# Optimization experiments

Hardware: AMD Instinct MI355X
Metric: run time of the kernel (lower is better)

Reference implementation:

```python
import jax, jax.numpy as jnp
import numpy as np

TOP_K = 500
CROP = (14, 14)


def crop_and_resize(img, nboxes, crop):
    # img: [H,W,C]; nboxes: [N,4] normalized (y1,x1,y2,x2); TF crop_and_resize semantics,
    # bilinear, extrapolation_value=0.
    H, W, C = img.shape
    ch, cw = crop
    y1, x1, y2, x2 = nboxes[:, 0], nboxes[:, 1], nboxes[:, 2], nboxes[:, 3]
    ty = jnp.arange(ch, dtype=img.dtype) / (ch - 1)  # [ch]
    tx = jnp.arange(cw, dtype=img.dtype) / (cw - 1)  # [cw]
    ys = (y1[:, None] + ty[None, :] * (y2 - y1)[:, None]) * (H - 1)  # [N,ch]
    xs = (x1[:, None] + tx[None, :] * (x2 - x1)[:, None]) * (W - 1)  # [N,cw]
    y0f = jnp.floor(ys); x0f = jnp.floor(xs)
    wy = (ys - y0f)[:, :, None, None]  # [N,ch,1,1]
    wx = (xs - x0f)[:, None, :, None]  # [N,1,cw,1]
    y0 = jnp.clip(y0f.astype(jnp.int32), 0, H - 1)
    y1i = jnp.clip(y0f.astype(jnp.int32) + 1, 0, H - 1)
    x0 = jnp.clip(x0f.astype(jnp.int32), 0, W - 1)
    x1i = jnp.clip(x0f.astype(jnp.int32) + 1, 0, W - 1)
    g = lambda yi, xi: img[yi[:, :, None], xi[:, None, :]]  # [N,ch,cw,C]
    out = ((1 - wy) * (1 - wx)) * g(y0, x0) + ((1 - wy) * wx) * g(y0, x1i) \
        + (wy * (1 - wx)) * g(y1i, x0) + (wy * wx) * g(y1i, x1i)
    my = (ys >= 0) & (ys <= H - 1)  # [N,ch]
    mx = (xs >= 0) & (xs <= W - 1)  # [N,cw]
    mask = (my[:, :, None] & mx[:, None, :])[..., None]
    return jnp.where(mask, out, jnp.zeros((), img.dtype))


def setup_inputs() -> dict:
    key = jax.random.key(0)
    ks = jax.random.split(key, 8)
    N, NC = 196416, 80
    image_shape = jnp.array([1, 1024, 1024, 3], dtype=jnp.int32)
    # boxes in pixel coords (x1,y1,x2,y2), within the 1024x1024 image
    boxes = jax.random.uniform(ks[0], (1, N, 4), dtype=jnp.float32) * 1024.0
    classification = jax.random.uniform(ks[1], (1, N, NC), dtype=jnp.float32)
    p3 = jax.random.normal(ks[2], (1, 128, 128, 256), dtype=jnp.float32)
    p4 = jax.random.normal(ks[3], (1, 64, 64, 256), dtype=jnp.float32)
    p5 = jax.random.normal(ks[4], (1, 32, 32, 256), dtype=jnp.float32)
    p6 = jax.random.normal(ks[5], (1, 16, 16, 256), dtype=jnp.float32)
    p7 = jax.random.normal(ks[6], (1, 8, 8, 256), dtype=jnp.float32)
    return {"image_shape": image_shape, "boxes": boxes, "classification": classification,
            "p3": p3, "p4": p4, "p5": p5, "p6": p6, "p7": p7}


def reference(image_shape, boxes, classification, p3, p4, p5, p6, p7):
    b = boxes[0]            # [N,4]
    c = classification[0]   # [N,NC]
    scores = jnp.max(c, axis=1)                       # [N]
    _, idx = jax.lax.top_k(scores, TOP_K)             # [top_k]
    b = b[idx]
    c = c[idx]
    h = image_shape[1].astype(jnp.float32)
    w = image_shape[2].astype(jnp.float32)
    x1, y1, x2, y2 = b[:, 0], b[:, 1], b[:, 2], b[:, 3]
    normed = jnp.stack([y1 / h, x1 / w, y2 / h, x2 / w], axis=1)  # [top_k,4]
    rois = jnp.concatenate(
        [crop_and_resize(f[0], normed, CROP) for f in (p3, p4, p5, p6, p7)], axis=-1)
    return b[None], c[None], rois[None]
```

## Files before the change

### kernel.cpp

```cpp
#include <hip/hip_runtime.h>

#define TOPK 500
#define NCLS 80
#define NPOS 196
#define NLEV 5
#define OUT_B_OFF 0
#define OUT_C_OFF 2000
#define OUT_R_OFF 42000

typedef float nfloat4 __attribute__((ext_vector_type(4)));
typedef unsigned long long u64;

#define SC_BLOCKS 768
#define SLICE     32
#define CUT       0x3F7FF000u
#define CAP_M     5632

#define WS_CNT    0
#define WS_TOP    4096
#define WS_BOXP   8192
#define WS_CAND   16384
#define WS_SCORES 262144
#define WS_FEAT   (1u << 20)
#define FEAT_PX   21824
#define BF16_BYTES ((size_t)FEAT_PX * 256 * 2)

__device__ inline unsigned short f2bf(float f) {
    unsigned u = __float_as_uint(f);
    return (unsigned short)((u + 0x7FFFu + ((u >> 16) & 1u)) >> 16);
}

__global__ __launch_bounds__(256) void k_prep(
    const float* __restrict__ cls, float* __restrict__ scores,
    int* __restrict__ candCnt, u64* __restrict__ cand, int N,
    const float* __restrict__ p3, const float* __restrict__ p4,
    const float* __restrict__ p5, const float* __restrict__ p6,
    const float* __restrict__ p7, ushort* __restrict__ dst) {
    int b = blockIdx.x;
    int t = threadIdx.x;
    if (b < SC_BLOCKS) {
        __shared__ int lcnt;
        __shared__ u64 stage[SLICE];
        if (t == 0) lcnt = 0;
        __syncthreads();
        int i = b * 256 + t;
        if (i < N) {
            const float4* p = (const float4*)(cls + (size_t)i * NCLS);
            float m = -1e30f;
#pragma unroll
            for (int k = 0; k < NCLS / 4; ++k) {
                float4 v = p[k];
                m = fmaxf(m, fmaxf(fmaxf(v.x, v.y), fmaxf(v.z, v.w)));
            }
            scores[i] = m;
            unsigned bits = __float_as_uint(m);
            if (bits >= CUT) {
                int p2 = atomicAdd(&lcnt, 1);
                if (p2 < SLICE) stage[p2] = ((u64)bits << 32) | (unsigned)(~i);
            }
        }
        __syncthreads();
        if (t == 0) candCnt[b] = lcnt;
        if (t < min(lcnt, SLICE)) cand[b * SLICE + t] = stage[t];
    } else {
        int i = (b - SC_BLOCKS) * 256 + t;
        const int n0 = 1048576, n1 = 262144, n2 = 65536, n3 = 16384;
        const float* src; int off;
        if (i < n0)               { src = p3; off = i; }
        else if (i < n0+n1)       { src = p4; off = i - n0; }
        else if (i < n0+n1+n2)    { src = p5; off = i - n0 - n1; }
        else if (i < n0+n1+n2+n3) { src = p6; off = i - n0 - n1 - n2; }
        else                      { src = p7; off = i - n0 - n1 - n2 - n3; }
        float4 v = ((const float4*)src)[off];
        ushort4 r;
        r.x = f2bf(v.x); r.y = f2bf(v.y); r.z = f2bf(v.z); r.w = f2bf(v.w);
        ((ushort4*)dst)[i] = r;
    }
}

__global__ __launch_bounds__(1024) void k_topk(
    const float* __restrict__ scores, int N,
    const int* __restrict__ candCnt, const u64* __restrict__ cand,
    const float* __restrict__ boxes, const float* __restrict__ cls,
    const int* __restrict__ ishape,
    int* __restrict__ topIdx, float* __restrict__ boxp, float* __restrict__ out) {
    __shared__ u64 dense[CAP_M];
    __shared__ int sv[768];
    __shared__ int hist[256];
    __shared__ int ss[256];
    __shared__ u64 key[1024];
    __shared__ int ordTop[TOPK];
    __shared__ int sBad, sCh, sK, nTot;
    __shared__ unsigned sAnd, sOr;
    int t = threadIdx.x;
    if (t == 0) { sBad = 0; nTot = 0; sAnd = 0xFFFFFFFFu; sOr = 0u; }
    key[t] = 0ull;
    int myv = 0;
    if (t < 768) {
        int c = candCnt[t];
        if (c > SLICE) atomicOr(&sBad, 1);
        myv = min(c, SLICE);
        sv[t] = myv;
    }
    __syncthreads();
    for (int o = 1; o < 1024; o <<= 1) {
        int x = 0;
        if (t < 768 && t >= o) x = sv[t - o];
        __syncthreads();
        if (t < 768 && t >= o) sv[t] += x;
        __syncthreads();
    }
    int M = sv[767];
    bool valid = (!sBad) && (M >= TOPK) && (M <= CAP_M);
    if (valid && t < 768) {
        int off = sv[t] - myv;
        for (int s = 0; s < myv; ++s) dense[off + s] = cand[t * SLICE + s];
    }
    __syncthreads();

    unsigned prefix = 0;
    int k = TOPK;
    if (valid) {
        unsigned ma = 0xFFFFFFFFu, mo = 0u;
        for (int q = t; q < M; q += 1024) {
            unsigned b = (unsigned)(dense[q] >> 32);
            ma &= b; mo |= b;
        }
        for (int o = 32; o; o >>= 1) { ma &= __shfl_down(ma, o); mo |= __shfl_down(mo, o); }
        if ((t & 63) == 0) { atomicAnd(&sAnd, ma); atomicOr(&sOr, mo); }
        __syncthreads();
        unsigned ga = sAnd, go = sOr;
        for (int p = 0; p < 4; ++p) {
            int shift = 24 - 8 * p;
            unsigned cA = (ga >> shift) & 255u, cO = (go >> shift) & 255u;
            if (cA == cO) { prefix |= cA << shift; continue; }
            unsigned mask = (p == 0) ? 0u : (0xFFFFFFFFu << (32 - 8 * p));
            if (t < 256) hist[t] = 0;
            __syncthreads();
            for (int q = t; q < M; q += 1024) {
                unsigned b = (unsigned)(dense[q] >> 32);
                if ((b & mask) == prefix) atomicAdd(&hist[(b >> shift) & 255u], 1);
            }
            __syncthreads();
            if (t < 256) ss[t] = hist[t];
            __syncthreads();
            for (int o = 1; o < 256; o <<= 1) {
                int v2 = 0;
                if (t < 256 && t + o < 256) v2 = ss[t + o];
                __syncthreads();
                if (t < 256) ss[t] += v2;
                __syncthreads();
            }
            if (t < 256 && ss[t] >= k && (t == 255 || ss[t + 1] < k)) {
                sCh = t; sK = k - ((t == 255) ? 0 : ss[t + 1]);
            }
            __syncthreads();
            prefix |= ((unsigned)sCh) << shift;
            k = sK;
            __syncthreads();
        }
        for (int q = t; q < M; q += 1024) {
            u64 kk = dense[q];
            if ((unsigned)(kk >> 32) >= prefix) {
                int p2 = atomicAdd(&nTot, 1);
                if (p2 < 1024) key[p2] = kk;
            }
        }
    } else {
        for (int p = 0; p < 4; ++p) {
            int shift = 24 - 8 * p;
            unsigned mask = (p == 0) ? 0u : (0xFFFFFFFFu << (32 - 8 * p));
            if (t < 256) hist[t] = 0;
            __syncthreads();
            for (int q = t; q < N; q += 1024) {
                unsigned b = __float_as_uint(scores[q]);
                if ((b & mask) == prefix) atomicAdd(&hist[(b >> shift) & 255u], 1);
            }
            __syncthreads();
            if (t < 256) ss[t] = hist[t];
            __syncthreads();
            for (int o = 1; o < 256; o <<= 1) {
                int v2 = 0;
                if (t < 256 && t + o < 256) v2 = ss[t + o];
                __syncthreads();
                if (t < 256) ss[t] += v2;
                __syncthreads();
            }
            if (t < 256 && ss[t] >= k && (t == 255 || ss[t + 1] < k)) {
                sCh = t; sK = k - ((t == 255) ? 0 : ss[t + 1]);
            }
            __syncthreads();
            prefix |= ((unsigned)sCh) << shift;
            k = sK;
            __syncthreads();
        }
        for (int q = t; q < N; q += 1024) {
            unsigned b = __float_as_uint(scores[q]);
            if (b >= prefix) {
                int p2 = atomicAdd(&nTot, 1);
                if (p2 < 1024) key[p2] = ((u64)b << 32) | (unsigned)(~q);
            }
        }
    }
    __syncthreads();
    float hf = (float)ishape[1], wf = (float)ishape[2];
    u64 me = key[t];
    if (me) {
        int r = 0;
        for (int j = 0; j < 1024; ++j) r += (key[j] > me);
        if (r < TOPK) {
            int idx = (int)(~(unsigned)(me & 0xFFFFFFFFull));
            ordTop[r] = idx;
            topIdx[r] = idx;
            float bx1 = boxes[idx * 4 + 0], by1 = boxes[idx * 4 + 1];
            float bx2 = boxes[idx * 4 + 2], by2 = boxes[idx * 4 + 3];
            nfloat4 bp;
            bp.x = by1 / hf; bp.y = bx1 / wf;
            bp.z = (by2 - by1) / hf; bp.w = (bx2 - bx1) / wf;
            *(nfloat4*)(boxp + 4 * r) = bp;
        }
    }
    __syncthreads();
    for (int e = t; e < TOPK * (NCLS + 4); e += 1024) {
        int j = e / (NCLS + 4);
        int k2 = e - j * (NCLS + 4);
        int idx = ordTop[j];
        if (k2 < 4) out[OUT_B_OFF + j * 4 + k2] = boxes[(size_t)idx * 4 + k2];
        else        out[OUT_C_OFF + j * NCLS + (k2 - 4)] = cls[(size_t)idx * NCLS + (k2 - 4)];
    }
}

template <int USE_BF16>
__global__ __launch_bounds__(256) void k_roi(
    const float* __restrict__ boxp, const int* __restrict__ topIdx,
    const ushort* __restrict__ feat,
    const float* __restrict__ f0, const float* __restrict__ f1,
    const float* __restrict__ f2, const float* __restrict__ f3,
    const float* __restrict__ f4,
    float* __restrict__ out) {
    const int lvlOff[5] = {0, 16384, 20480, 21504, 21760};
    int nwg = gridDim.x;
    int q = nwg >> 3, r = nwg & 7;
    int orig = blockIdx.x;
    int xcd = orig & 7, i8 = orig >> 3;
    int wg = (xcd < r ? xcd * (q + 1) : r * (q + 1) + (xcd - r) * q) + i8;
    int P  = wg * 4 + (threadIdx.x >> 6);
    int c4 = threadIdx.x & 63;
    int j = P / NPOS;
    int pos = P - j * NPOS;
    int y = pos / 14, x = pos - (pos / 14) * 14;
    nfloat4 bp = *(const nfloat4*)(boxp + 4 * j);
    float ty = (float)y / 13.0f;
    float tx = (float)x / 13.0f;
    const float* fm[5] = {f0, f1, f2, f3, f4};
    float* o = out + OUT_R_OFF + (size_t)P * (NLEV * 256);
#pragma unroll
    for (int l = 0; l < NLEV; ++l) {
        int H = 128 >> l;
        float Hm1 = (float)(H - 1);
        float ys = (bp.x + ty * bp.z) * Hm1;
        float xs = (bp.y + tx * bp.w) * Hm1;
        float y0f = floorf(ys), x0f = floorf(xs);
        float wy = ys - y0f, wx = xs - x0f;
        int y0  = min(max((int)y0f, 0), H - 1);
        int y1c = min(max((int)y0f + 1, 0), H - 1);
        int x0  = min(max((int)x0f, 0), H - 1);
        int x1c = min(max((int)x0f + 1, 0), H - 1);
        bool valid = (ys >= 0.0f) && (ys <= Hm1) && (xs >= 0.0f) && (xs <= Hm1);
        float w00 = (1.0f - wy) * (1.0f - wx);
        float w01 = (1.0f - wy) * wx;
        float w10 = wy * (1.0f - wx);
        float w11 = wy * wx;
        nfloat4 res;
        if (USE_BF16) {
            const ushort* base = feat + ((size_t)lvlOff[l] << 8);
            ushort4 a = ((const ushort4*)(base + ((size_t)(y0  * H + x0 ) << 8)))[c4];
            ushort4 b = ((const ushort4*)(base + ((size_t)(y0  * H + x1c) << 8)))[c4];
            ushort4 c = ((const ushort4*)(base + ((size_t)(y1c * H + x0 ) << 8)))[c4];
            ushort4 d = ((const ushort4*)(base + ((size_t)(y1c * H + x1c) << 8)))[c4];
#define BF(u) __uint_as_float(((unsigned)(u)) << 16)
            res.x = w00 * BF(a.x) + w01 * BF(b.x) + w10 * BF(c.x) + w11 * BF(d.x);
            res.y = w00 * BF(a.y) + w01 * BF(b.y) + w10 * BF(c.y) + w11 * BF(d.y);
            res.z = w00 * BF(a.z) + w01 * BF(b.z) + w10 * BF(c.z) + w11 * BF(d.z);
            res.w = w00 * BF(a.w) + w01 * BF(b.w) + w10 * BF(c.w) + w11 * BF(d.w);
#undef BF
        } else {
            const float* f = fm[l];
            float4 a = ((const float4*)(f + ((size_t)(y0  * H + x0 ) << 8)))[c4];
            float4 b = ((const float4*)(f + ((size_t)(y0  * H + x1c) << 8)))[c4];
            float4 c = ((const float4*)(f + ((size_t)(y1c * H + x0 ) << 8)))[c4];
            float4 d = ((const float4*)(f + ((size_t)(y1c * H + x1c) << 8)))[c4];
            res.x = w00 * a.x + w01 * b.x + w10 * c.x + w11 * d.x;
            res.y = w00 * a.y + w01 * b.y + w10 * c.y + w11 * d.y;
            res.z = w00 * a.z + w01 * b.z + w10 * c.z + w11 * d.z;
            res.w = w00 * a.w + w01 * b.w + w10 * c.w + w11 * d.w;
        }
        if (!valid) { res.x = 0.f; res.y = 0.f; res.z = 0.f; res.w = 0.f; }
        __builtin_nontemporal_store(res, (nfloat4*)(o + l * 256) + c4);
    }
}

extern "C" void kernel_launch(void* const* d_in, const int* in_sizes, int n_in,
                              void* d_out, int out_size, void* d_ws, size_t ws_size,
                              hipStream_t stream) {
    const int*   ishape = (const int*)d_in[0];
    const float* boxes  = (const float*)d_in[1];
    const float* cls    = (const float*)d_in[2];
    const float* p3     = (const float*)d_in[3];
    const float* p4     = (const float*)d_in[4];
    const float* p5     = (const float*)d_in[5];
    const float* p6     = (const float*)d_in[6];
    const float* p7     = (const float*)d_in[7];
    float* out = (float*)d_out;

    int N = in_sizes[2] / NCLS;

    char* ws = (char*)d_ws;
    int*    candCnt = (int*)(ws + WS_CNT);
    int*    topIdx  = (int*)(ws + WS_TOP);
    float*  boxp    = (float*)(ws + WS_BOXP);
    u64*    cand    = (u64*)(ws + WS_CAND);
    float*  scores  = (float*)(ws + WS_SCORES);
    ushort* feat    = (ushort*)(ws + WS_FEAT);

    bool useBf16 = ws_size >= (size_t)WS_FEAT + BF16_BYTES;

    hipLaunchKernelGGL(k_prep, dim3(useBf16 ? SC_BLOCKS + 5456 : SC_BLOCKS), dim3(256), 0, stream,
                       cls, scores, candCnt, cand, N, p3, p4, p5, p6, p7, feat);
    hipLaunchKernelGGL(k_topk, dim3(1), dim3(1024), 0, stream,
                       scores, N, candCnt, cand, boxes, cls, ishape, topIdx, boxp, out);
    if (useBf16)
        hipLaunchKernelGGL((k_roi<1>), dim3(TOPK * NPOS / 4), dim3(256), 0, stream,
                           boxp, topIdx, feat, p3, p4, p5, p6, p7, out);
    else
        hipLaunchKernelGGL((k_roi<0>), dim3(TOPK * NPOS / 4), dim3(256), 0, stream,
                           boxp, topIdx, feat, p3, p4, p5, p6, p7, out);
}
```

Measured before the change: 144.4 us.

## Overlap bf16 feature conversion with single-block top-k and batch ROI loads

Moves the fp32-to-bf16 feature conversion out of the score kernel and into extra blocks of the top-k launch, so the conversion runs alongside the single-block top-k selection instead of before it. The score kernel now uses four threads per row with shuffle reductions, which coalesces its reads of the class scores. The ROI kernel issues all gathers for the five levels before doing any interpolation, to expose more memory-level parallelism. This raises register pressure in the ROI kernel, and the 1024-thread top-k launch now shares the GPU with many conversion blocks that may delay the critical block.

After: 143.5 us. Within noise of the previous version (-0.6%).

```diff
diff --git a/kernel.cpp b/kernel.cpp
--- a/kernel.cpp
+++ b/kernel.cpp
@@ -25,6 +25,9 @@
 #define FEAT_PX   21824
 #define BF16_BYTES ((size_t)FEAT_PX * 256 * 2)
 
+#define CVT_TOTAL 1396736
+#define CVT_BLOCKS (CVT_TOTAL / 1024)
+
 __device__ inline unsigned short f2bf(float f) {
     unsigned u = __float_as_uint(f);
     return (unsigned short)((u + 0x7FFFu + ((u >> 16) & 1u)) >> 16);
@@ -32,38 +35,53 @@
 
 __global__ __launch_bounds__(256) void k_prep(
     const float* __restrict__ cls, float* __restrict__ scores,
-    int* __restrict__ candCnt, u64* __restrict__ cand, int N,
-    const float* __restrict__ p3, const float* __restrict__ p4,
-    const float* __restrict__ p5, const float* __restrict__ p6,
-    const float* __restrict__ p7, ushort* __restrict__ dst) {
-    int b = blockIdx.x;
-    int t = threadIdx.x;
-    if (b < SC_BLOCKS) {
-        __shared__ int lcnt;
-        __shared__ u64 stage[SLICE];
-        if (t == 0) lcnt = 0;
-        __syncthreads();
-        int i = b * 256 + t;
+    int* __restrict__ candCnt, u64* __restrict__ cand, int N) {
+    __shared__ int lcnt;
+    __shared__ u64 stage[SLICE];
+    int b = blockIdx.x, t = threadIdx.x;
+    if (t == 0) lcnt = 0;
+    __syncthreads();
+    int g = t >> 2, q = t & 3;
+#pragma unroll
+    for (int it = 0; it < 4; ++it) {
+        int i = b * 256 + it * 64 + g;
         if (i < N) {
             const float4* p = (const float4*)(cls + (size_t)i * NCLS);
             float m = -1e30f;
 #pragma unroll
-            for (int k = 0; k < NCLS / 4; ++k) {
-                float4 v = p[k];
+            for (int j2 = 0; j2 < 5; ++j2) {
+                float4 v = p[j2 * 4 + q];
                 m = fmaxf(m, fmaxf(fmaxf(v.x, v.y), fmaxf(v.z, v.w)));
             }
-            scores[i] = m;
-            unsigned bits = __float_as_uint(m);
-            if (bits >= CUT) {
-                int p2 = atomicAdd(&lcnt, 1);
-                if (p2 < SLICE) stage[p2] = ((u64)bits << 32) | (unsigned)(~i);
-            }
-        }
-        __syncthreads();
-        if (t == 0) candCnt[b] = lcnt;
-        if (t < min(lcnt, SLICE)) cand[b * SLICE + t] = stage[t];
-    } else {
-        int i = (b - SC_BLOCKS) * 256 + t;
+            m = fmaxf(m, __shfl_xor(m, 1));
+            m = fmaxf(m, __shfl_xor(m, 2));
+            if (q == 0) {
+                scores[i] = m;
+                unsigned bits = __float_as_uint(m);
+                if (bits >= CUT) {
+                    int p2 = atomicAdd(&lcnt, 1);
+                    if (p2 < SLICE) stage[p2] = ((u64)bits << 32) | (unsigned)(~i);
+                }
+            }
+        }
+    }
+    __syncthreads();
+    if (t == 0) candCnt[b] = lcnt;
+    if (t < min(lcnt, SLICE)) cand[b * SLICE + t] = stage[t];
+}
+
+__global__ __launch_bounds__(1024) void k_topk(
+    const float* __restrict__ scores, int N,
+    const int* __restrict__ candCnt, const u64* __restrict__ cand,
+    const float* __restrict__ boxes, const float* __restrict__ cls,
+    const int* __restrict__ ishape,
+    int* __restrict__ topIdx, float* __restrict__ boxp, float* __restrict__ out,
+    const float* __restrict__ p3, const float* __restrict__ p4,
+    const float* __restrict__ p5, const float* __restrict__ p6,
+    const float* __restrict__ p7, ushort* __restrict__ fdst) {
+    int t = threadIdx.x;
+    if (blockIdx.x != 0) {
+        int i = (int)(blockIdx.x - 1) * 1024 + t;
         const int n0 = 1048576, n1 = 262144, n2 = 65536, n3 = 16384;
         const float* src; int off;
         if (i < n0)               { src = p3; off = i; }
@@ -74,16 +92,9 @@
         float4 v = ((const float4*)src)[off];
         ushort4 r;
         r.x = f2bf(v.x); r.y = f2bf(v.y); r.z = f2bf(v.z); r.w = f2bf(v.w);
-        ((ushort4*)dst)[i] = r;
-    }
-}
-
-__global__ __launch_bounds__(1024) void k_topk(
-    const float* __restrict__ scores, int N,
-    const int* __restrict__ candCnt, const u64* __restrict__ cand,
-    const float* __restrict__ boxes, const float* __restrict__ cls,
-    const int* __restrict__ ishape,
-    int* __restrict__ topIdx, float* __restrict__ boxp, float* __restrict__ out) {
+        ((ushort4*)fdst)[i] = r;
+        return;
+    }
     __shared__ u64 dense[CAP_M];
     __shared__ int sv[768];
     __shared__ int hist[256];
@@ -92,7 +103,6 @@
     __shared__ int ordTop[TOPK];
     __shared__ int sBad, sCh, sK, nTot;
     __shared__ unsigned sAnd, sOr;
-    int t = threadIdx.x;
     if (t == 0) { sBad = 0; nTot = 0; sAnd = 0xFFFFFFFFu; sOr = 0u; }
     key[t] = 0ull;
     int myv = 0;
@@ -254,6 +264,11 @@
     float tx = (float)x / 13.0f;
     const float* fm[5] = {f0, f1, f2, f3, f4};
     float* o = out + OUT_R_OFF + (size_t)P * (NLEV * 256);
+
+    nfloat4 wgt[5];
+    bool vld[5];
+    ushort4 A[5], B[5], C[5], D[5];
+    float4 FA[5], FB[5], FC[5], FD[5];
 #pragma unroll
     for (int l = 0; l < NLEV; ++l) {
         int H = 128 >> l;
@@ -266,36 +281,43 @@
         int y1c = min(max((int)y0f + 1, 0), H - 1);
         int x0  = min(max((int)x0f, 0), H - 1);
         int x1c = min(max((int)x0f + 1, 0), H - 1);
-        bool valid = (ys >= 0.0f) && (ys <= Hm1) && (xs >= 0.0f) && (xs <= Hm1);
-        float w00 = (1.0f - wy) * (1.0f - wx);
-        float w01 = (1.0f - wy) * wx;
-        float w10 = wy * (1.0f - wx);
-        float w11 = wy * wx;
+        vld[l] = (ys >= 0.0f) && (ys <= Hm1) && (xs >= 0.0f) && (xs <= Hm1);
+        wgt[l].x = (1.0f - wy) * (1.0f - wx);
+        wgt[l].y = (1.0f - wy) * wx;
+        wgt[l].z = wy * (1.0f - wx);
+        wgt[l].w = wy * wx;
+        if (USE_BF16) {
+            const ushort* base = feat + ((size_t)lvlOff[l] << 8);
+            A[l] = ((const ushort4*)(base + ((size_t)(y0  * H + x0 ) << 8)))[c4];
+            B[l] = ((const ushort4*)(base + ((size_t)(y0  * H + x1c) << 8)))[c4];
+            C[l] = ((const ushort4*)(base + ((size_t)(y1c * H + x0 ) << 8)))[c4];
+            D[l] = ((const ushort4*)(base + ((size_t)(y1c * H + x1c) << 8)))[c4];
+        } else {
+            const float* f = fm[l];
+            FA[l] = ((const float4*)(f + ((size_t)(y0  * H + x0 ) << 8)))[c4];
+            FB[l] = ((const float4*)(f + ((size_t)(y0  * H + x1c) << 8)))[c4];
+            FC[l] = ((const float4*)(f + ((size_t)(y1c * H + x0 ) << 8)))[c4];
+            FD[l] = ((const float4*)(f + ((size_t)(y1c * H + x1c) << 8)))[c4];
+        }
+    }
+#pragma unroll
+    for (int l = 0; l < NLEV; ++l) {
+        float w00 = wgt[l].x, w01 = wgt[l].y, w10 = wgt[l].z, w11 = wgt[l].w;
         nfloat4 res;
         if (USE_BF16) {
-            const ushort* base = feat + ((size_t)lvlOff[l] << 8);
-            ushort4 a = ((const ushort4*)(base + ((size_t)(y0  * H + x0 ) << 8)))[c4];
-            ushort4 b = ((const ushort4*)(base + ((size_t)(y0  * H + x1c) << 8)))[c4];
-            ushort4 c = ((const ushort4*)(base + ((size_t)(y1c * H + x0 ) << 8)))[c4];
-            ushort4 d = ((const ushort4*)(base + ((size_t)(y1c * H + x1c) << 8)))[c4];
 #define BF(u) __uint_as_float(((unsigned)(u)) << 16)
-            res.x = w00 * BF(a.x) + w01 * BF(b.x) + w10 * BF(c.x) + w11 * BF(d.x);
-            res.y = w00 * BF(a.y) + w01 * BF(b.y) + w10 * BF(c.y) + w11 * BF(d.y);
-            res.z = w00 * BF(a.z) + w01 * BF(b.z) + w10 * BF(c.z) + w11 * BF(d.z);
-            res.w = w00 * BF(a.w) + w01 * BF(b.w) + w10 * BF(c.w) + w11 * BF(d.w);
+            res.x = w00 * BF(A[l].x) + w01 * BF(B[l].x) + w10 * BF(C[l].x) + w11 * BF(D[l].x);
+            res.y = w00 * BF(A[l].y) + w01 * BF(B[l].y) + w10 * BF(C[l].y) + w11 * BF(D[l].y);
+            res.z = w00 * BF(A[l].z) + w01 * BF(B[l].z) + w10 * BF(C[l].z) + w11 * BF(D[l].z);
+            res.w = w00 * BF(A[l].w) + w01 * BF(B[l].w) + w10 * BF(C[l].w) + w11 * BF(D[l].w);
 #undef BF
         } else {
-            const float* f = fm[l];
-            float4 a = ((const float4*)(f + ((size_t)(y0  * H + x0 ) << 8)))[c4];
-            float4 b = ((const float4*)(f + ((size_t)(y0  * H + x1c) << 8)))[c4];
-            float4 c = ((const float4*)(f + ((size_t)(y1c * H + x0 ) << 8)))[c4];
-            float4 d = ((const float4*)(f + ((size_t)(y1c * H + x1c) << 8)))[c4];
-            res.x = w00 * a.x + w01 * b.x + w10 * c.x + w11 * d.x;
-            res.y = w00 * a.y + w01 * b.y + w10 * c.y + w11 * d.y;
-            res.z = w00 * a.z + w01 * b.z + w10 * c.z + w11 * d.z;
-            res.w = w00 * a.w + w01 * b.w + w10 * c.w + w11 * d.w;
-        }
-        if (!valid) { res.x = 0.f; res.y = 0.f; res.z = 0.f; res.w = 0.f; }
+            res.x = w00 * FA[l].x + w01 * FB[l].x + w10 * FC[l].x + w11 * FD[l].x;
+            res.y = w00 * FA[l].y + w01 * FB[l].y + w10 * FC[l].y + w11 * FD[l].y;
+            res.z = w00 * FA[l].z + w01 * FB[l].z + w10 * FC[l].z + w11 * FD[l].z;
+            res.w = w00 * FA[l].w + w01 * FB[l].w + w10 * FC[l].w + w11 * FD[l].w;
+        }
+        if (!vld[l]) { res.x = 0.f; res.y = 0.f; res.z = 0.f; res.w = 0.f; }
         __builtin_nontemporal_store(res, (nfloat4*)(o + l * 256) + c4);
     }
 }
@@ -325,10 +347,11 @@
 
     bool useBf16 = ws_size >= (size_t)WS_FEAT + BF16_BYTES;
 
-    hipLaunchKernelGGL(k_prep, dim3(useBf16 ? SC_BLOCKS + 5456 : SC_BLOCKS), dim3(256), 0, stream,
-                       cls, scores, candCnt, cand, N, p3, p4, p5, p6, p7, feat);
-    hipLaunchKernelGGL(k_topk, dim3(1), dim3(1024), 0, stream,
-                       scores, N, candCnt, cand, boxes, cls, ishape, topIdx, boxp, out);
+    hipLaunchKernelGGL(k_prep, dim3(SC_BLOCKS), dim3(256), 0, stream,
+                       cls, scores, candCnt, cand, N);
+    hipLaunchKernelGGL(k_topk, dim3(useBf16 ? 1 + CVT_BLOCKS : 1), dim3(1024), 0, stream,
+                       scores, N, candCnt, cand, boxes, cls, ishape, topIdx, boxp, out,
+                       p3, p4, p5, p6, p7, feat);
     if (useBf16)
         hipLaunchKernelGGL((k_roi<1>), dim3(TOPK * NPOS / 4), dim3(256), 0, stream,
                            boxp, topIdx, feat, p3, p4, p5, p6, p7, out);
```
